# Kernel optimization log

Hardware: AMD Instinct MI355X
Metric: run time of the kernel (lower is better)

Reference implementation:

```python
import jax, jax.numpy as jnp
import numpy as np

B, F, N = 128, 256, 2000

def setup_inputs() -> dict:
    key = jax.random.key(0)
    ks = jax.random.split(key, 10)
    s = 0.05
    return {
        'nfeature': jax.random.normal(ks[0], (B, F, N, 1), jnp.float32),
        'last_current': jax.random.randint(ks[1], (B, 2), 0, N, jnp.int32),
        'Wg': jax.random.normal(ks[2], (F, F), jnp.float32) * s,
        'bg': jax.random.normal(ks[3], (F,), jnp.float32) * s,
        'Wnode': jax.random.normal(ks[4], (3 * F, F), jnp.float32) * s,
        'bnode': jax.random.normal(ks[5], (3 * F,), jnp.float32) * s,
        'Wlc': jax.random.normal(ks[6], (F, 2 * F), jnp.float32) * s,
        'blc': jax.random.normal(ks[7], (F,), jnp.float32) * s,
        'Wproj': jax.random.normal(ks[8], (F, F), jnp.float32) * s,
        'bproj': jax.random.normal(ks[9], (F,), jnp.float32) * s,
    }

def reference(nfeature, last_current, Wg, bg, Wnode, bnode, Wlc, blc, Wproj, bproj):
    # nfeature: [B, F, N, 1]
    x = nfeature[..., 0]                                  # [B, F, N]
    f = x.shape[1]
    scale = 1.0 / jnp.sqrt(jnp.asarray(f, x.dtype))
    # global fixed query: max over nodes then Linear
    glb = jnp.max(x, axis=2)                              # [B, F]
    Q = glb @ Wg.T + bg                                   # [B, F]
    # node embeddings via 1x1 conv == channel GEMM, split into K, V, logit_K
    kvl = jnp.einsum('bfn,gf->bgn', x, Wnode) + bnode[None, :, None]  # [B, 3F, N]
    K, V, Klog = jnp.split(kvl, 3, axis=1)                # each [B, F, N]
    # gather last/current city features
    lc = jnp.take_along_axis(x, last_current[:, None, :], axis=2)     # [B, F, 2]
    context = jnp.concatenate([lc[:, :, 0], lc[:, :, 1]], axis=1)     # [B, 2F]
    cQ = context @ Wlc.T + blc + Q                        # [B, F]
    # attention: single query over N keys
    ucj = jnp.einsum('bf,bfn->bn', cQ, K) * scale         # [B, N]
    attn = jax.nn.softmax(ucj, axis=1)
    nc = jnp.einsum('bn,bfn->bf', attn, V)                # [B, F]
    nc = nc @ Wproj.T + bproj                             # [B, F]
    logits = jnp.einsum('bf,bfn->bn', nc, Klog) * scale   # [B, N]
    return jnp.tanh(logits) * 10.0
```

## Files before the change

### kernel.cpp

```cpp
#include <hip/hip_runtime.h>
#include <hip/hip_fp16.h>
#include <math.h>

#define BB 128
#define FF 256
#define NN 2000

typedef float f32x4 __attribute__((ext_vector_type(4)));
union H8 { f32x4 v; __half2 h[4]; };

__global__ __launch_bounds__(256) void k_convmax(const float* __restrict__ x,
                                                 __half* __restrict__ xh,
                                                 float* __restrict__ glb) {
    int row  = (blockIdx.x << 2) | (threadIdx.x >> 6);
    int lane = threadIdx.x & 63;
    const f32x4* src = (const f32x4*)(x + (size_t)row * NN);
    f32x4*       dst = (f32x4*)(xh + (size_t)row * NN);
    float m = -INFINITY;
    for (int i = lane; i < 250; i += 64) {
        f32x4 a = __builtin_nontemporal_load(src + 2 * i);
        f32x4 b = __builtin_nontemporal_load(src + 2 * i + 1);
        m = fmaxf(m, fmaxf(fmaxf(a.x, a.y), fmaxf(a.z, a.w)));
        m = fmaxf(m, fmaxf(fmaxf(b.x, b.y), fmaxf(b.z, b.w)));
        H8 o;
        o.h[0] = __floats2half2_rn(a.x, a.y);
        o.h[1] = __floats2half2_rn(a.z, a.w);
        o.h[2] = __floats2half2_rn(b.x, b.y);
        o.h[3] = __floats2half2_rn(b.z, b.w);
        dst[i] = o.v;
    }
#pragma unroll
    for (int off = 32; off; off >>= 1) m = fmaxf(m, __shfl_xor(m, off));
    if (!lane) glb[row] = m;
}

__global__ __launch_bounds__(256) void k_prep(
    const float* __restrict__ x, const int* __restrict__ lc,
    const float* __restrict__ glb,
    const float* __restrict__ Wg, const float* __restrict__ bg,
    const float* __restrict__ Wnode, const float* __restrict__ bnode,
    const float* __restrict__ Wlc, const float* __restrict__ blc,
    float* __restrict__ cK, float* __restrict__ cK0)
{
    int b = blockIdx.x;
    int f = threadIdx.x;
    __shared__ float s_glb[FF], s_ctx[2 * FF], s_cQ[FF], s_red[FF];
    const float* xb = x + (size_t)b * FF * NN;
    s_glb[f] = glb[b * FF + f];
    int l0 = lc[2 * b], l1 = lc[2 * b + 1];
    s_ctx[f]      = xb[(size_t)f * NN + l0];
    s_ctx[FF + f] = xb[(size_t)f * NN + l1];
    __syncthreads();
    const float* wg = Wg + (size_t)f * FF;
    float q0 = 0, q1 = 0, q2 = 0, q3 = 0;
    for (int j = 0; j < FF; j += 4) {
        q0 = fmaf(wg[j],     s_glb[j],     q0);
        q1 = fmaf(wg[j + 1], s_glb[j + 1], q1);
        q2 = fmaf(wg[j + 2], s_glb[j + 2], q2);
        q3 = fmaf(wg[j + 3], s_glb[j + 3], q3);
    }
    const float* wl = Wlc + (size_t)f * 2 * FF;
    for (int j = 0; j < 2 * FF; j += 4) {
        q0 = fmaf(wl[j],     s_ctx[j],     q0);
        q1 = fmaf(wl[j + 1], s_ctx[j + 1], q1);
        q2 = fmaf(wl[j + 2], s_ctx[j + 2], q2);
        q3 = fmaf(wl[j + 3], s_ctx[j + 3], q3);
    }
    float cq = bg[f] + blc[f] + ((q0 + q1) + (q2 + q3));
    s_cQ[f]  = cq;
    s_red[f] = cq * bnode[f];
    __syncthreads();
    float c0 = 0, c1 = 0;
    for (int g = 0; g < FF; g += 2) {
        c0 = fmaf(s_cQ[g],     Wnode[(size_t)g * FF + f],       c0);
        c1 = fmaf(s_cQ[g + 1], Wnode[(size_t)(g + 1) * FF + f], c1);
    }
    cK[b * FF + f] = c0 + c1;
    for (int s = 128; s > 0; s >>= 1) {
        if (f < s) s_red[f] += s_red[f + s];
        __syncthreads();
    }
    if (f == 0) cK0[b] = s_red[0];
}

__global__ __launch_bounds__(256) void k_attn(
    const __half* __restrict__ xh,
    const float* __restrict__ cK, const float* __restrict__ cK0,
    float* __restrict__ y_part8, float* __restrict__ m_part,
    float* __restrict__ s_part)
{
    int b = blockIdx.x >> 2, s = blockIdx.x & 3;
    int tid = threadIdx.x, w = tid >> 6, lane = tid & 63;
    __shared__ float s_cK[FF];
    __shared__ float s_buf[4][512];
    __shared__ float s_p[512];
    __shared__ float s_red[8];
    s_cK[tid] = cK[b * FF + tid];
    __syncthreads();

    int n0 = s << 9;
    int nbase = n0 + (lane << 3);
    bool valid = nbase < NN;
    int cb = lane << 3;

    float a0 = 0, a1 = 0, a2 = 0, a3 = 0, a4 = 0, a5 = 0, a6 = 0, a7 = 0;
    const __half* rp = xh + (size_t)(b * FF + (w << 6)) * NN + nbase;
    if (valid) {
#pragma unroll 4
        for (int fi = 0; fi < 64; ++fi) {
            H8 hv; hv.v = *(const f32x4*)(rp + (size_t)fi * NN);
            float c = s_cK[(w << 6) + fi];
            float2 q0 = __half22float2(hv.h[0]);
            float2 q1 = __half22float2(hv.h[1]);
            float2 q2 = __half22float2(hv.h[2]);
            float2 q3 = __half22float2(hv.h[3]);
            a0 = fmaf(c, q0.x, a0); a1 = fmaf(c, q0.y, a1);
            a2 = fmaf(c, q1.x, a2); a3 = fmaf(c, q1.y, a3);
            a4 = fmaf(c, q2.x, a4); a5 = fmaf(c, q2.y, a5);
            a6 = fmaf(c, q3.x, a6); a7 = fmaf(c, q3.y, a7);
        }
    }
    s_buf[w][cb + 0] = a0; s_buf[w][cb + 1] = a1;
    s_buf[w][cb + 2] = a2; s_buf[w][cb + 3] = a3;
    s_buf[w][cb + 4] = a4; s_buf[w][cb + 5] = a5;
    s_buf[w][cb + 6] = a6; s_buf[w][cb + 7] = a7;
    __syncthreads();

    const float scale = 0.0625f;
    float k0 = cK0[b];
    float uu0, uu1;
    {
        int c0 = tid, c1 = tid + 256;
        float t0 = s_buf[0][c0] + s_buf[1][c0] + s_buf[2][c0] + s_buf[3][c0];
        float t1 = s_buf[0][c1] + s_buf[1][c1] + s_buf[2][c1] + s_buf[3][c1];
        uu0 = (n0 + c0 < NN) ? (t0 + k0) * scale : -INFINITY;
        uu1 = (n0 + c1 < NN) ? (t1 + k0) * scale : -INFINITY;
    }
    float m = fmaxf(uu0, uu1);
#pragma unroll
    for (int off = 32; off; off >>= 1) m = fmaxf(m, __shfl_xor(m, off));
    if (!lane) s_red[w] = m;
    __syncthreads();
    float M = fmaxf(fmaxf(s_red[0], s_red[1]), fmaxf(s_red[2], s_red[3]));
    float e0 = (uu0 > -INFINITY) ? __expf(uu0 - M) : 0.f;
    float e1 = (uu1 > -INFINITY) ? __expf(uu1 - M) : 0.f;
    float ss = e0 + e1;
#pragma unroll
    for (int off = 32; off; off >>= 1) ss += __shfl_xor(ss, off);
    __syncthreads();
    s_p[tid]       = e0;
    s_p[tid + 256] = e1;
    if (!lane) s_red[4 + w] = ss;
    __syncthreads();
    if (!tid) {
        m_part[(b << 2) + s] = M;
        s_part[(b << 2) + s] = s_red[4] + s_red[5] + s_red[6] + s_red[7];
    }

    float4 pa = *(const float4*)&s_p[cb];
    float4 pc = *(const float4*)&s_p[cb + 4];
    float* yout = y_part8 + ((size_t)((b << 2) + s)) * 2048 + (w << 9);
    int row = lane >> 3, k = lane & 7;
    for (int g = 0; g < 8; ++g) {
        float part[8];
#pragma unroll
        for (int r = 0; r < 8; ++r) {
            float acc = 0.f;
            if (valid) {
                H8 hv; hv.v = *(const f32x4*)(rp + (size_t)((g << 3) + r) * NN);
                float2 q0 = __half22float2(hv.h[0]);
                float2 q1 = __half22float2(hv.h[1]);
                float2 q2 = __half22float2(hv.h[2]);
                float2 q3 = __half22float2(hv.h[3]);
                acc = fmaf(pa.x, q0.x, acc); acc = fmaf(pa.y, q0.y, acc);
                acc = fmaf(pa.z, q1.x, acc); acc = fmaf(pa.w, q1.y, acc);
                acc = fmaf(pc.x, q2.x, acc); acc = fmaf(pc.y, q2.y, acc);
                acc = fmaf(pc.z, q3.x, acc); acc = fmaf(pc.w, q3.y, acc);
            }
            part[r] = acc;
        }
#pragma unroll
        for (int r = 0; r < 8; ++r) s_buf[w][(r << 6) + lane] = part[r];
        __syncthreads();
        const float* src = &s_buf[w][(row << 6) + (k << 3)];
        float4 aa = *(const float4*)src;
        float4 bb = *(const float4*)(src + 4);
        float sum8 = ((aa.x + aa.y) + (aa.z + aa.w)) + ((bb.x + bb.y) + (bb.z + bb.w));
        yout[(g << 6) + lane] = sum8;
        __syncthreads();
    }
}

__global__ __launch_bounds__(256) void k_dense(
    const float* __restrict__ y_part8, const float* __restrict__ m_part,
    const float* __restrict__ s_part,
    const float* __restrict__ Wnode, const float* __restrict__ bnode,
    const float* __restrict__ Wproj, const float* __restrict__ bproj,
    float* __restrict__ cL, float* __restrict__ cL0)
{
    int b = blockIdx.x;
    int f = threadIdx.x;
    int wid = f >> 6, lane = f & 63;
    __shared__ float s_y[FF], s_v[FF], s_red[4];

    float m0 = m_part[(b << 2)],     m1 = m_part[(b << 2) + 1];
    float m2 = m_part[(b << 2) + 2], m3 = m_part[(b << 2) + 3];
    float M = fmaxf(fmaxf(m0, m1), fmaxf(m2, m3));
    float w0 = __expf(m0 - M), w1 = __expf(m1 - M);
    float w2 = __expf(m2 - M), w3 = __expf(m3 - M);
    float S = s_part[(b << 2)] * w0 + s_part[(b << 2) + 1] * w1 +
              s_part[(b << 2) + 2] * w2 + s_part[(b << 2) + 3] * w3;
    float invS = 1.0f / S;
    const float* yb = y_part8 + ((size_t)b << 13);
    float wgt[4] = {w0, w1, w2, w3};
    float acc = 0.f;
#pragma unroll
    for (int s = 0; s < 4; ++s) {
        float4 aa = *(const float4*)(yb + (s << 11) + (f << 3));
        float4 bb = *(const float4*)(yb + (s << 11) + (f << 3) + 4);
        acc += wgt[s] * (((aa.x + aa.y) + (aa.z + aa.w)) + ((bb.x + bb.y) + (bb.z + bb.w)));
    }
    s_y[f] = acc * invS;
    __syncthreads();

    const float* wv = Wnode + (size_t)(FF + f) * FF;
    float a0 = 0, a1 = 0, a2 = 0, a3 = 0;
    for (int j = 0; j < FF; j += 4) {
        a0 = fmaf(wv[j],     s_y[j],     a0);
        a1 = fmaf(wv[j + 1], s_y[j + 1], a1);
        a2 = fmaf(wv[j + 2], s_y[j + 2], a2);
        a3 = fmaf(wv[j + 3], s_y[j + 3], a3);
    }
    s_v[f] = bnode[FF + f] + ((a0 + a1) + (a2 + a3));
    __syncthreads();
    const float* wp = Wproj + (size_t)f * FF;
    a0 = 0; a1 = 0; a2 = 0; a3 = 0;
    for (int j = 0; j < FF; j += 4) {
        a0 = fmaf(wp[j],     s_v[j],     a0);
        a1 = fmaf(wp[j + 1], s_v[j + 1], a1);
        a2 = fmaf(wp[j + 2], s_v[j + 2], a2);
        a3 = fmaf(wp[j + 3], s_v[j + 3], a3);
    }
    float nc2 = bproj[f] + ((a0 + a1) + (a2 + a3));
    __syncthreads();
    s_v[f] = nc2;
    __syncthreads();
    float c0 = 0, c1 = 0;
    for (int g = 0; g < FF; g += 2) {
        c0 = fmaf(s_v[g],     Wnode[(size_t)(2 * FF + g) * FF + f],     c0);
        c1 = fmaf(s_v[g + 1], Wnode[(size_t)(2 * FF + g + 1) * FF + f], c1);
    }
    cL[b * FF + f] = c0 + c1;
    float t = nc2 * bnode[2 * FF + f];
#pragma unroll
    for (int off = 32; off; off >>= 1) t += __shfl_xor(t, off);
    if (!lane) s_red[wid] = t;
    __syncthreads();
    if (!f) cL0[b] = s_red[0] + s_red[1] + s_red[2] + s_red[3];
}

__global__ __launch_bounds__(256) void k_logits(const __half* __restrict__ xh,
                                                const float* __restrict__ cL,
                                                const float* __restrict__ cL0,
                                                float* __restrict__ out)
{
    int b = blockIdx.x >> 2, s = blockIdx.x & 3;
    int tid = threadIdx.x, w = tid >> 6, lane = tid & 63;
    __shared__ float s_cL[FF];
    __shared__ float s_acc[4][512];
    s_cL[tid] = cL[b * FF + tid];
    __syncthreads();
    int n0 = s << 9;
    int nbase = n0 + (lane << 3);
    float a0 = 0, a1 = 0, a2 = 0, a3 = 0, a4 = 0, a5 = 0, a6 = 0, a7 = 0;
    if (nbase < NN) {
        const __half* rp = xh + (size_t)(b * FF + (w << 6)) * NN + nbase;
#pragma unroll 4
        for (int fi = 0; fi < 64; ++fi) {
            H8 hv; hv.v = *(const f32x4*)rp;
            rp += NN;
            float c = s_cL[(w << 6) + fi];
            float2 q0 = __half22float2(hv.h[0]);
            float2 q1 = __half22float2(hv.h[1]);
            float2 q2 = __half22float2(hv.h[2]);
            float2 q3 = __half22float2(hv.h[3]);
            a0 = fmaf(c, q0.x, a0); a1 = fmaf(c, q0.y, a1);
            a2 = fmaf(c, q1.x, a2); a3 = fmaf(c, q1.y, a3);
            a4 = fmaf(c, q2.x, a4); a5 = fmaf(c, q2.y, a5);
            a6 = fmaf(c, q3.x, a6); a7 = fmaf(c, q3.y, a7);
        }
    }
    int cb = lane << 3;
    s_acc[w][cb + 0] = a0; s_acc[w][cb + 1] = a1;
    s_acc[w][cb + 2] = a2; s_acc[w][cb + 3] = a3;
    s_acc[w][cb + 4] = a4; s_acc[w][cb + 5] = a5;
    s_acc[w][cb + 6] = a6; s_acc[w][cb + 7] = a7;
    __syncthreads();
    float cl0 = cL0[b];
    const float scale = 0.0625f;
#pragma unroll
    for (int j = 0; j < 2; ++j) {
        int c = tid + (j << 8);
        int n = n0 + c;
        if (n < NN) {
            float l = (s_acc[0][c] + s_acc[1][c] + s_acc[2][c] + s_acc[3][c] + cl0) * scale;
            out[(size_t)b * NN + n] = tanhf(l) * 10.f;
        }
    }
}

extern "C" void kernel_launch(void* const* d_in, const int* in_sizes, int n_in,
                              void* d_out, int out_size, void* d_ws, size_t ws_size,
                              hipStream_t stream) {
    const float* x     = (const float*)d_in[0];
    const int*   lc    = (const int*)d_in[1];
    const float* Wg    = (const float*)d_in[2];
    const float* bg    = (const float*)d_in[3];
    const float* Wnode = (const float*)d_in[4];
    const float* bnode = (const float*)d_in[5];
    const float* Wlc   = (const float*)d_in[6];
    const float* blc   = (const float*)d_in[7];
    const float* Wproj = (const float*)d_in[8];
    const float* bproj = (const float*)d_in[9];
    float* out = (float*)d_out;

    float* ws      = (float*)d_ws;
    float* glb     = ws + 0;
    float* cK      = ws + 40960;
    float* cK0     = ws + 81920;
    float* m_part  = ws + 82432;
    float* s_part  = ws + 83456;
    float* cL      = ws + 84480;
    float* cL0     = ws + 117248;
    float* y_part8 = ws + 118272;
    __half* xh     = (__half*)(ws + (2 << 20));

    k_convmax<<<BB * FF / 4, 256, 0, stream>>>(x, xh, glb);
    k_prep   <<<BB, 256, 0, stream>>>(x, lc, glb, Wg, bg, Wnode, bnode, Wlc, blc, cK, cK0);
    k_attn   <<<BB * 4, 256, 0, stream>>>(xh, cK, cK0, y_part8, m_part, s_part);
    k_dense  <<<BB, 256, 0, stream>>>(y_part8, m_part, s_part, Wnode, bnode, Wproj, bproj, cL, cL0);
    k_logits <<<BB * 4, 256, 0, stream>>>(xh, cL, cL0, out);
}
```

Baseline: 201.9 us.

## Double block size in attn and logits kernels, batch loads, drop intra-warp syncs

k_attn and k_logits now run 512 threads (8 waves) per block, and each wave handles 32 feature rows instead of 64. This doubles the waves in flight to hide memory latency over the fp16 copy of x. The dot-product loops now issue 8 independent 16-byte loads before consuming them, which adds memory-level parallelism. The __syncthreads around the per-wave shared-buffer reduction in the V pass are removed because each wave only touches its own slice. The cost is more LDS per block and more partial sums to combine in the cross-wave reduction.

Result: faster. 196.1 us (-2.9%).

```diff
diff --git a/kernel.cpp b/kernel.cpp
--- a/kernel.cpp
+++ b/kernel.cpp
@@ -83,7 +83,7 @@
     if (f == 0) cK0[b] = s_red[0];
 }
 
-__global__ __launch_bounds__(256) void k_attn(
+__global__ __launch_bounds__(512) void k_attn(
     const __half* __restrict__ xh,
     const float* __restrict__ cK, const float* __restrict__ cK0,
     float* __restrict__ y_part8, float* __restrict__ m_part,
@@ -92,32 +92,39 @@
     int b = blockIdx.x >> 2, s = blockIdx.x & 3;
     int tid = threadIdx.x, w = tid >> 6, lane = tid & 63;
     __shared__ float s_cK[FF];
-    __shared__ float s_buf[4][512];
+    __shared__ float s_buf[8][512];
     __shared__ float s_p[512];
-    __shared__ float s_red[8];
-    s_cK[tid] = cK[b * FF + tid];
+    __shared__ float s_red[8], s_red2[8];
+    if (tid < FF) s_cK[tid] = cK[b * FF + tid];
     __syncthreads();
 
     int n0 = s << 9;
     int nbase = n0 + (lane << 3);
     bool valid = nbase < NN;
     int cb = lane << 3;
+    const __half* rp = xh + (size_t)(b * FF + (w << 5)) * NN + nbase;
 
     float a0 = 0, a1 = 0, a2 = 0, a3 = 0, a4 = 0, a5 = 0, a6 = 0, a7 = 0;
-    const __half* rp = xh + (size_t)(b * FF + (w << 6)) * NN + nbase;
     if (valid) {
-#pragma unroll 4
-        for (int fi = 0; fi < 64; ++fi) {
-            H8 hv; hv.v = *(const f32x4*)(rp + (size_t)fi * NN);
-            float c = s_cK[(w << 6) + fi];
-            float2 q0 = __half22float2(hv.h[0]);
-            float2 q1 = __half22float2(hv.h[1]);
-            float2 q2 = __half22float2(hv.h[2]);
-            float2 q3 = __half22float2(hv.h[3]);
-            a0 = fmaf(c, q0.x, a0); a1 = fmaf(c, q0.y, a1);
-            a2 = fmaf(c, q1.x, a2); a3 = fmaf(c, q1.y, a3);
-            a4 = fmaf(c, q2.x, a4); a5 = fmaf(c, q2.y, a5);
-            a6 = fmaf(c, q3.x, a6); a7 = fmaf(c, q3.y, a7);
+#pragma unroll
+        for (int g = 0; g < 4; ++g) {
+            f32x4 hv[8];
+#pragma unroll
+            for (int r = 0; r < 8; ++r)
+                hv[r] = *(const f32x4*)(rp + (size_t)((g << 3) + r) * NN);
+#pragma unroll
+            for (int r = 0; r < 8; ++r) {
+                H8 u; u.v = hv[r];
+                float c = s_cK[(w << 5) + (g << 3) + r];
+                float2 q0 = __half22float2(u.h[0]);
+                float2 q1 = __half22float2(u.h[1]);
+                float2 q2 = __half22float2(u.h[2]);
+                float2 q3 = __half22float2(u.h[3]);
+                a0 = fmaf(c, q0.x, a0); a1 = fmaf(c, q0.y, a1);
+                a2 = fmaf(c, q1.x, a2); a3 = fmaf(c, q1.y, a3);
+                a4 = fmaf(c, q2.x, a4); a5 = fmaf(c, q2.y, a5);
+                a6 = fmaf(c, q3.x, a6); a7 = fmaf(c, q3.y, a7);
+            }
         }
     }
     s_buf[w][cb + 0] = a0; s_buf[w][cb + 1] = a1;
@@ -128,50 +135,49 @@
 
     const float scale = 0.0625f;
     float k0 = cK0[b];
-    float uu0, uu1;
-    {
-        int c0 = tid, c1 = tid + 256;
-        float t0 = s_buf[0][c0] + s_buf[1][c0] + s_buf[2][c0] + s_buf[3][c0];
-        float t1 = s_buf[0][c1] + s_buf[1][c1] + s_buf[2][c1] + s_buf[3][c1];
-        uu0 = (n0 + c0 < NN) ? (t0 + k0) * scale : -INFINITY;
-        uu1 = (n0 + c1 < NN) ? (t1 + k0) * scale : -INFINITY;
-    }
-    float m = fmaxf(uu0, uu1);
+    float u = 0.f;
+#pragma unroll
+    for (int ww = 0; ww < 8; ++ww) u += s_buf[ww][tid];
+    float uu = (n0 + tid < NN) ? (u + k0) * scale : -INFINITY;
+    float m = uu;
 #pragma unroll
     for (int off = 32; off; off >>= 1) m = fmaxf(m, __shfl_xor(m, off));
     if (!lane) s_red[w] = m;
     __syncthreads();
-    float M = fmaxf(fmaxf(s_red[0], s_red[1]), fmaxf(s_red[2], s_red[3]));
-    float e0 = (uu0 > -INFINITY) ? __expf(uu0 - M) : 0.f;
-    float e1 = (uu1 > -INFINITY) ? __expf(uu1 - M) : 0.f;
-    float ss = e0 + e1;
+    float M = s_red[0];
+#pragma unroll
+    for (int ww = 1; ww < 8; ++ww) M = fmaxf(M, s_red[ww]);
+    float e = (uu > -INFINITY) ? __expf(uu - M) : 0.f;
+    s_p[tid] = e;
+    float ss = e;
 #pragma unroll
     for (int off = 32; off; off >>= 1) ss += __shfl_xor(ss, off);
-    __syncthreads();
-    s_p[tid]       = e0;
-    s_p[tid + 256] = e1;
-    if (!lane) s_red[4 + w] = ss;
+    if (!lane) s_red2[w] = ss;
     __syncthreads();
     if (!tid) {
+        float S = 0.f;
+#pragma unroll
+        for (int ww = 0; ww < 8; ++ww) S += s_red2[ww];
         m_part[(b << 2) + s] = M;
-        s_part[(b << 2) + s] = s_red[4] + s_red[5] + s_red[6] + s_red[7];
+        s_part[(b << 2) + s] = S;
     }
 
     float4 pa = *(const float4*)&s_p[cb];
     float4 pc = *(const float4*)&s_p[cb + 4];
-    float* yout = y_part8 + ((size_t)((b << 2) + s)) * 2048 + (w << 9);
+    float* yout = y_part8 + (size_t)((b << 2) + s) * 2048 + (w << 8);
     int row = lane >> 3, k = lane & 7;
-    for (int g = 0; g < 8; ++g) {
+#pragma unroll
+    for (int g = 0; g < 4; ++g) {
         float part[8];
 #pragma unroll
         for (int r = 0; r < 8; ++r) {
             float acc = 0.f;
             if (valid) {
-                H8 hv; hv.v = *(const f32x4*)(rp + (size_t)((g << 3) + r) * NN);
-                float2 q0 = __half22float2(hv.h[0]);
-                float2 q1 = __half22float2(hv.h[1]);
-                float2 q2 = __half22float2(hv.h[2]);
-                float2 q3 = __half22float2(hv.h[3]);
+                H8 u2; u2.v = *(const f32x4*)(rp + (size_t)((g << 3) + r) * NN);
+                float2 q0 = __half22float2(u2.h[0]);
+                float2 q1 = __half22float2(u2.h[1]);
+                float2 q2 = __half22float2(u2.h[2]);
+                float2 q3 = __half22float2(u2.h[3]);
                 acc = fmaf(pa.x, q0.x, acc); acc = fmaf(pa.y, q0.y, acc);
                 acc = fmaf(pa.z, q1.x, acc); acc = fmaf(pa.w, q1.y, acc);
                 acc = fmaf(pc.x, q2.x, acc); acc = fmaf(pc.y, q2.y, acc);
@@ -181,13 +187,11 @@
         }
 #pragma unroll
         for (int r = 0; r < 8; ++r) s_buf[w][(r << 6) + lane] = part[r];
-        __syncthreads();
-        const float* src = &s_buf[w][(row << 6) + (k << 3)];
-        float4 aa = *(const float4*)src;
-        float4 bb = *(const float4*)(src + 4);
-        float sum8 = ((aa.x + aa.y) + (aa.z + aa.w)) + ((bb.x + bb.y) + (bb.z + bb.w));
-        yout[(g << 6) + lane] = sum8;
-        __syncthreads();
+        const float* srcp = &s_buf[w][(row << 6) + (k << 3)];
+        float4 aa = *(const float4*)srcp;
+        float4 bb = *(const float4*)(srcp + 4);
+        yout[(g << 6) + lane] =
+            ((aa.x + aa.y) + (aa.z + aa.w)) + ((bb.x + bb.y) + (bb.z + bb.w));
     }
 }
 
@@ -259,7 +263,7 @@
     if (!f) cL0[b] = s_red[0] + s_red[1] + s_red[2] + s_red[3];
 }
 
-__global__ __launch_bounds__(256) void k_logits(const __half* __restrict__ xh,
+__global__ __launch_bounds__(512) void k_logits(const __half* __restrict__ xh,
                                                 const float* __restrict__ cL,
                                                 const float* __restrict__ cL0,
                                                 float* __restrict__ out)
@@ -267,45 +271,48 @@
     int b = blockIdx.x >> 2, s = blockIdx.x & 3;
     int tid = threadIdx.x, w = tid >> 6, lane = tid & 63;
     __shared__ float s_cL[FF];
-    __shared__ float s_acc[4][512];
-    s_cL[tid] = cL[b * FF + tid];
+    __shared__ float s_acc[8][512];
+    if (tid < FF) s_cL[tid] = cL[b * FF + tid];
     __syncthreads();
     int n0 = s << 9;
     int nbase = n0 + (lane << 3);
+    bool valid = nbase < NN;
+    int cb = lane << 3;
+    const __half* rp = xh + (size_t)(b * FF + (w << 5)) * NN + nbase;
     float a0 = 0, a1 = 0, a2 = 0, a3 = 0, a4 = 0, a5 = 0, a6 = 0, a7 = 0;
-    if (nbase < NN) {
-        const __half* rp = xh + (size_t)(b * FF + (w << 6)) * NN + nbase;
-#pragma unroll 4
-        for (int fi = 0; fi < 64; ++fi) {
-            H8 hv; hv.v = *(const f32x4*)rp;
-            rp += NN;
-            float c = s_cL[(w << 6) + fi];
-            float2 q0 = __half22float2(hv.h[0]);
-            float2 q1 = __half22float2(hv.h[1]);
-            float2 q2 = __half22float2(hv.h[2]);
-            float2 q3 = __half22float2(hv.h[3]);
-            a0 = fmaf(c, q0.x, a0); a1 = fmaf(c, q0.y, a1);
-            a2 = fmaf(c, q1.x, a2); a3 = fmaf(c, q1.y, a3);
-            a4 = fmaf(c, q2.x, a4); a5 = fmaf(c, q2.y, a5);
-            a6 = fmaf(c, q3.x, a6); a7 = fmaf(c, q3.y, a7);
+    if (valid) {
+#pragma unroll
+        for (int g = 0; g < 4; ++g) {
+            f32x4 hv[8];
+#pragma unroll
+            for (int r = 0; r < 8; ++r)
+                hv[r] = *(const f32x4*)(rp + (size_t)((g << 3) + r) * NN);
+#pragma unroll
+            for (int r = 0; r < 8; ++r) {
+                H8 u; u.v = hv[r];
+                float c = s_cL[(w << 5) + (g << 3) + r];
+                float2 q0 = __half22float2(u.h[0]);
+                float2 q1 = __half22float2(u.h[1]);
+                float2 q2 = __half22float2(u.h[2]);
+                float2 q3 = __half22float2(u.h[3]);
+                a0 = fmaf(c, q0.x, a0); a1 = fmaf(c, q0.y, a1);
+                a2 = fmaf(c, q1.x, a2); a3 = fmaf(c, q1.y, a3);
+                a4 = fmaf(c, q2.x, a4); a5 = fmaf(c, q2.y, a5);
+                a6 = fmaf(c, q3.x, a6); a7 = fmaf(c, q3.y, a7);
+            }
         }
     }
-    int cb = lane << 3;
     s_acc[w][cb + 0] = a0; s_acc[w][cb + 1] = a1;
     s_acc[w][cb + 2] = a2; s_acc[w][cb + 3] = a3;
     s_acc[w][cb + 4] = a4; s_acc[w][cb + 5] = a5;
     s_acc[w][cb + 6] = a6; s_acc[w][cb + 7] = a7;
     __syncthreads();
-    float cl0 = cL0[b];
-    const float scale = 0.0625f;
-#pragma unroll
-    for (int j = 0; j < 2; ++j) {
-        int c = tid + (j << 8);
-        int n = n0 + c;
-        if (n < NN) {
-            float l = (s_acc[0][c] + s_acc[1][c] + s_acc[2][c] + s_acc[3][c] + cl0) * scale;
-            out[(size_t)b * NN + n] = tanhf(l) * 10.f;
-        }
+    int n = n0 + tid;
+    if (n < NN) {
+        float t = 0.f;
+#pragma unroll
+        for (int ww = 0; ww < 8; ++ww) t += s_acc[ww][tid];
+        out[(size_t)b * NN + n] = tanhf((t + cL0[b]) * 0.0625f) * 10.f;
     }
 }
 
@@ -337,7 +344,7 @@
 
     k_convmax<<<BB * FF / 4, 256, 0, stream>>>(x, xh, glb);
     k_prep   <<<BB, 256, 0, stream>>>(x, lc, glb, Wg, bg, Wnode, bnode, Wlc, blc, cK, cK0);
-    k_attn   <<<BB * 4, 256, 0, stream>>>(xh, cK, cK0, y_part8, m_part, s_part);
+    k_attn   <<<BB * 4, 512, 0, stream>>>(xh, cK, cK0, y_part8, m_part, s_part);
     k_dense  <<<BB, 256, 0, stream>>>(y_part8, m_part, s_part, Wnode, bnode, Wproj, bproj, cL, cL0);
-    k_logits <<<BB * 4, 256, 0, stream>>>(xh, cL, cL0, out);
-}
+    k_logits <<<BB * 4, 512, 0, stream>>>(xh, cL, cL0, out);
+}
```
